# Kernel tuning notes

Hardware: AMD Instinct MI355X
Metric: run time of the kernel (lower is better)

The kernel has to match this reference:

```python
import jax, jax.numpy as jnp
import numpy as np

B, T, E = 4, 2048, 1024
H, HS = 16, 64

def setup_inputs() -> dict:
    key = jax.random.key(0)
    ks = jax.random.split(key, 6)
    return {
        "x": jax.random.normal(ks[0], (B, T, E), dtype=jnp.float32),
        "Wq": jax.random.normal(ks[1], (H, E, HS), dtype=jnp.float32) * 0.02,
        "Wk": jax.random.normal(ks[2], (H, E, HS), dtype=jnp.float32) * 0.02,
        "Wv": jax.random.normal(ks[3], (H, E, HS), dtype=jnp.float32) * 0.02,
        "proj_w": jax.random.normal(ks[4], (E, H * HS), dtype=jnp.float32) * 0.02,
        "proj_b": jax.random.normal(ks[5], (E,), dtype=jnp.float32) * 0.02,
    }

def reference(x, Wq, Wk, Wv, proj_w, proj_b):
    b, t, e = x.shape
    h, _, hs = Wq.shape
    # NOTE: original uses .view() (raw reshape, not transpose) from [b,t,h,hs]
    # to [h,b,t,hs]; we replicate that exactly for faithfulness.
    q = jnp.einsum('bxy,iyk->bxik', x, Wq).reshape(h, b, t, hs)
    k = jnp.einsum('bxy,iyk->bxik', x, Wk).reshape(h, b, t, hs)
    v = jnp.einsum('bxy,iyk->bxik', x, Wv).reshape(h, b, t, hs)
    # scores: [h, b, t, t], scaled by 1/sqrt(head_size)
    wei = jnp.einsum('hbqd,hbkd->hbqk', q, k) * (hs ** -0.5)
    causal = jnp.tril(jnp.ones((t, t), dtype=bool))  # [t, t]
    wei = jnp.where(causal, wei, -jnp.inf)
    wei = jax.nn.softmax(wei, axis=-1)  # dropout is identity in eval
    out = jnp.einsum('hbqk,hbkd->hbqd', wei, v)
    # raw reshape [h,b,t,hs] -> [b,t,h*hs], matching torch .view()
    out = out.reshape(b, t, h * hs)
    out = out @ proj_w.T + proj_b  # nn.Linear
    return out
```

## Files before the change

### kernel.cpp

```cpp
#include <hip/hip_runtime.h>

typedef unsigned short u16;
typedef __attribute__((ext_vector_type(8))) __bf16 bf16x8;
typedef __attribute__((ext_vector_type(4))) float f32x4;
typedef __attribute__((ext_vector_type(16))) float f32x16;
typedef __attribute__((ext_vector_type(4))) unsigned short ushort4v;
typedef __attribute__((ext_vector_type(2))) unsigned uint2v;

__device__ __forceinline__ u16 f2bf(float f) {
  unsigned u = __builtin_bit_cast(unsigned, f);
  u += 0x7fffu + ((u >> 16) & 1u);
  return (u16)(u >> 16);
}

__device__ __forceinline__ float exp2_hw(float x) {
  float r; asm("v_exp_f32 %0, %1" : "=v"(r) : "v"(x)); return r;
}
__device__ __forceinline__ unsigned cvt_pk_bf16(float a, float b) {
  unsigned r; asm("v_cvt_pk_bf16_f32 %0, %1, %2" : "=v"(r) : "v"(a), "v"(b)); return r;
}

__device__ __forceinline__ void gload_lds16(const void* g, void* l) {
  __builtin_amdgcn_global_load_lds(
      (__attribute__((address_space(1))) void*)g,
      (__attribute__((address_space(3))) void*)l, 16, 0, 0);
}

__device__ __forceinline__ void BAR() {
  asm volatile("" ::: "memory");
  __builtin_amdgcn_s_barrier();
  asm volatile("" ::: "memory");
}

#define MFMA16(a, b, c) __builtin_amdgcn_mfma_f32_16x16x32_bf16(a, b, c, 0, 0, 0)
#define MFMA32(a, b, c) __builtin_amdgcn_mfma_f32_32x32x16_bf16(a, b, c, 0, 0, 0)

#define QSCALE 0.1803368801111204f


__global__ __launch_bounds__(256)
void prep_kernel(const float* __restrict__ x, const float* __restrict__ Wq,
                 const float* __restrict__ Wk, const float* __restrict__ Wv,
                 const float* __restrict__ pw, u16* __restrict__ Xb,
                 u16* __restrict__ Wcat, u16* __restrict__ PWt) {
  const int b = blockIdx.x, tid = threadIdx.x;
  if (b < 8192) {
    int i = b * 256 + tid;
    float4 v = ((const float4*)x)[i];
    union { u16 u[4]; uint2 v2; } r;
    r.u[0] = f2bf(v.x); r.u[1] = f2bf(v.y); r.u[2] = f2bf(v.z); r.u[3] = f2bf(v.w);
    ((uint2*)Xb)[i] = r.v2;
  } else if (b < 8960) {
    __shared__ u16 lds[64 * 68];
    int bb = b - 8192;
    int sel = bb >> 8, rem = bb & 255;
    int h = rem >> 4, e0 = (rem & 15) * 64;
    const float* W = (sel == 0) ? Wq : (sel == 1) ? Wk : Wv;
    const float* src = W + ((size_t)h * 1024 + e0) * 64;
#pragma unroll
    for (int i = 0; i < 4; i++) {
      int idx = i * 1024 + tid * 4;
      int e = idx >> 6, hs = idx & 63;
      float4 v = *(const float4*)&src[idx];
      u16* d = &lds[e * 68 + hs];
      d[0] = f2bf(v.x); d[1] = f2bf(v.y); d[2] = f2bf(v.z); d[3] = f2bf(v.w);
    }
    __syncthreads();
#pragma unroll
    for (int i = 0; i < 2; i++) {
      int u = i * 256 + tid;
      int hs = u >> 3, ec = u & 7;
      union { u16 q[8]; uint4 v; } ou;
#pragma unroll
      for (int e = 0; e < 8; e++) ou.q[e] = lds[(ec * 8 + e) * 68 + hs];
      size_t n = (size_t)sel * 1024 + h * 64 + hs;
      *(uint4*)&Wcat[n * 1024 + e0 + ec * 8] = ou.v;
    }
  } else {
    int i = (b - 8960) * 256 + tid;
    float4 v = ((const float4*)pw)[i];
    union { u16 u[4]; uint2 v2; } r;
    r.u[0] = f2bf(v.x); r.u[1] = f2bf(v.y); r.u[2] = f2bf(v.z); r.u[3] = f2bf(v.w);
    ((uint2*)PWt)[i] = r.v2;
  }
}


template<int OUT_BF16>
__global__ __launch_bounds__(512, 2)
void gemm3b(const u16* __restrict__ A, const u16* __restrict__ BT,
            void* __restrict__ Cout, const float* __restrict__ bias,
            int M, int N, int K, int qcols) {
  __shared__ u16 a_lds[3][128 * 64];
  __shared__ u16 b_lds[3][256 * 64];
  const int xcd = blockIdx.x & 7;
  const int local = blockIdx.x >> 3;
  const int by = xcd * 8 + (local & 7);
  const int bx = local >> 3;
  const int tid = threadIdx.x;
  const int lane = tid & 63;
  const int w = tid >> 6;
  const int wr = w >> 2, wc = w & 3;
  const int mBase = by * 128, nBase = bx * 256;
  const int l15 = lane & 15, l4 = lane >> 4;
  const int nkt = K >> 6;

  f32x4 acc[4][4] = {};

  auto STAGE_A = [&](int s, int kt) {
#pragma unroll
    for (int j = 0; j < 2; j++) {
      int e = j * 4096 + tid * 8;
      int row = e >> 6;
      int c = ((e >> 3) & 7) ^ (row & 7);
      gload_lds16(A + (size_t)(mBase + row) * K + kt * 64 + c * 8, &a_lds[s][e]);
    }
  };
  auto STAGE_B = [&](int s, int kt) {
#pragma unroll
    for (int j = 0; j < 4; j++) {
      int e = j * 4096 + tid * 8;
      int row = e >> 6;
      int c = ((e >> 3) & 7) ^ (row & 7);
      gload_lds16(BT + (size_t)(nBase + row) * K + kt * 64 + c * 8, &b_lds[s][e]);
    }
  };

  STAGE_A(0, 0); STAGE_B(0, 0);
  STAGE_A(1, 1); STAGE_B(1, 1);
  asm volatile("s_waitcnt vmcnt(6)" ::: "memory");
  BAR();

  int s0 = 0, s1 = 1, s2 = 2;
  for (int t = 0; t < nkt; t++) {
    const int t2 = (t + 2 < nkt) ? t + 2 : t + 2 - nkt;
    bf16x8 AF[4][2], BF[2][2];

#pragma unroll
    for (int m = 0; m < 4; m++) {
      int row = wr * 64 + m * 16 + l15;
#pragma unroll
      for (int ks = 0; ks < 2; ks++) {
        int ch = (ks * 4 + l4) ^ (row & 7);
        AF[m][ks] = *(const bf16x8*)&a_lds[s0][row * 64 + ch * 8];
      }
    }
#pragma unroll
    for (int n = 0; n < 2; n++) {
      int row = wc * 64 + n * 16 + l15;
#pragma unroll
      for (int ks = 0; ks < 2; ks++) {
        int ch = (ks * 4 + l4) ^ (row & 7);
        BF[n][ks] = *(const bf16x8*)&b_lds[s0][row * 64 + ch * 8];
      }
    }
    STAGE_A(s2, t2);
    BAR();
    __builtin_amdgcn_s_setprio(1);
#pragma unroll
    for (int m = 0; m < 4; m++)
#pragma unroll
      for (int n = 0; n < 2; n++) {
        acc[m][n] = MFMA16(AF[m][0], BF[n][0], acc[m][n]);
        acc[m][n] = MFMA16(AF[m][1], BF[n][1], acc[m][n]);
      }
    __builtin_amdgcn_s_setprio(0);

#pragma unroll
    for (int n = 0; n < 2; n++) {
      int row = wc * 64 + 32 + n * 16 + l15;
#pragma unroll
      for (int ks = 0; ks < 2; ks++) {
        int ch = (ks * 4 + l4) ^ (row & 7);
        BF[n][ks] = *(const bf16x8*)&b_lds[s0][row * 64 + ch * 8];
      }
    }
    STAGE_B(s2, t2);
    BAR();
    __builtin_amdgcn_s_setprio(1);
#pragma unroll
    for (int m = 0; m < 4; m++)
#pragma unroll
      for (int n = 0; n < 2; n++) {
        acc[m][2 + n] = MFMA16(AF[m][0], BF[n][0], acc[m][2 + n]);
        acc[m][2 + n] = MFMA16(AF[m][1], BF[n][1], acc[m][2 + n]);
      }
    __builtin_amdgcn_s_setprio(0);

    asm volatile("s_waitcnt vmcnt(6)" ::: "memory");
    BAR();
    int tmp = s0; s0 = s1; s1 = s2; s2 = tmp;
  }

#pragma unroll
  for (int mi = 0; mi < 4; mi++) {
    int row = mBase + wr * 64 + mi * 16 + l4 * 4;
#pragma unroll
    for (int ni = 0; ni < 4; ni++) {
      int col = nBase + wc * 64 + ni * 16 + l15;
      float scl = (col < qcols) ? QSCALE : 1.f;
#pragma unroll
      for (int j = 0; j < 4; j++) {
        float v = acc[mi][ni][j];
        if (OUT_BF16) {
          ((u16*)Cout)[(size_t)(row + j) * N + col] = f2bf(v * scl);
        } else {
          ((float*)Cout)[(size_t)(row + j) * N + col] = v + bias[col];
        }
      }
    }
  }
}


__global__ __launch_bounds__(256)
void vt_build(const u16* __restrict__ qkv, u16* __restrict__ vt) {
  __shared__ u16 lds[64 * 66];
  const int hb = blockIdx.x >> 5, tc = blockIdx.x & 31;
  const int t0 = tc * 64, tid = threadIdx.x;
#pragma unroll
  for (int i = 0; i < 2; i++) {
    int idx = i * 2048 + tid * 8;
    int tl = idx >> 6, d0 = idx & 63;
    int r = hb * 2048 + t0 + tl;
    const u16* src = &qkv[(size_t)(r >> 4) * 3072 + 2048 + (r & 15) * 64 + d0];
    uint4 v = *(const uint4*)src;
    u16* dst = &lds[tl * 66 + d0];
    *(unsigned*)(dst + 0) = v.x; *(unsigned*)(dst + 2) = v.y;
    *(unsigned*)(dst + 4) = v.z; *(unsigned*)(dst + 6) = v.w;
  }
  __syncthreads();
#pragma unroll
  for (int i = 0; i < 2; i++) {
    int idx = i * 2048 + tid * 8;
    int d = idx >> 6, tl0 = idx & 63;
    union { u16 u[8]; uint4 v; } ou;
#pragma unroll
    for (int e = 0; e < 8; e++) ou.u[e] = lds[(tl0 + e) * 66 + d];
    *(uint4*)&vt[(size_t)hb * 131072 + (size_t)d * 2048 + t0 + tl0] = ou.v;
  }
}


__global__ __launch_bounds__(256)
void attn_kernel(const u16* __restrict__ qkv, const u16* __restrict__ vtg,
                 u16* __restrict__ att) {
  __shared__ u16 k_lds[2][64 * 64];
  __shared__ u16 v_lds[2][64 * 64];

  const int xcd = blockIdx.x & 7;
  const int c = blockIdx.x >> 3;
  const int hb = xcd * 8 + (c & 7);
  const int qb = 15 - (c >> 3);
  const int tid = threadIdx.x;
  const int lane = tid & 63, w = tid >> 6;
  const int l31 = lane & 31, l5 = lane >> 5;
  const int qbase = qb * 128 + w * 32;
  const int nkt = 2 * qb + 2;

  bf16x8 qf[4];
  {
    int t = qbase + l31;
    int r = hb * 2048 + t;
    size_t base = (size_t)(r >> 4) * 3072 + (r & 15) * 64;
#pragma unroll
    for (int d = 0; d < 4; d++)
      qf[d] = *(const bf16x8*)&qkv[base + d * 16 + l5 * 8];
  }

  f32x16 o0 = {}, o1 = {};
  float lp = 0.f;

  auto STAGE = [&](int buf, int kt) {
#pragma unroll
    for (int i = 0; i < 2; i++) {
      int U = i * 2048 + tid * 8;
      int row = U >> 6;
      int chunk = ((U >> 3) & 7) ^ (row & 7);
      int rK = hb * 2048 + kt * 64 + row;
      gload_lds16(&qkv[(size_t)(rK >> 4) * 3072 + 1024 + (rK & 15) * 64 + chunk * 8],
                  &k_lds[buf][U]);
    }
#pragma unroll
    for (int i = 0; i < 2; i++) {
      int U = i * 2048 + tid * 8;
      int row = U >> 6;
      int chunk = ((U >> 3) & 7) ^ (row & 7);
      gload_lds16(&vtg[(size_t)hb * 131072 + (size_t)row * 2048 + kt * 64 + chunk * 8],
                  &v_lds[buf][U]);
    }
  };

  STAGE(0, 0);
  asm volatile("s_waitcnt vmcnt(0)" ::: "memory");
  BAR();

  for (int kt = 0; kt < nkt; kt++) {
    if (kt + 1 < nkt) STAGE((kt + 1) & 1, kt + 1);
    const int cur = kt & 1;
    const bool active = (kt * 64 <= qbase + 31);
    if (active) {
      const bool full = (kt * 64 + 63 <= qbase);
      const int q = qbase + l31;
#pragma unroll
      for (int kb = 0; kb < 2; kb++) {
        int krow = kb * 32 + l31;
        int ksw = krow & 7;
        f32x16 st = {};
        __builtin_amdgcn_s_setprio(1);
#pragma unroll
        for (int t = 0; t < 4; t++) {
          bf16x8 kf = *(const bf16x8*)&k_lds[cur][krow * 64 + ((t * 2 + l5) ^ ksw) * 8];
          st = MFMA32(kf, qf[t], st);
        }
        __builtin_amdgcn_s_setprio(0);
        float p[16];
#pragma unroll
        for (int r = 0; r < 16; r++) {
          float v = st[r];
          if (!full) {
            int k = kt * 64 + kb * 32 + (r & 3) + 8 * (r >> 2) + 4 * l5;
            v = (k > q) ? -INFINITY : v;
          }
          p[r] = exp2_hw(v);
          lp += p[r];
        }
#pragma unroll
        for (int kc = 0; kc < 2; kc++) {
          unsigned w0 = cvt_pk_bf16(p[kc * 8 + 0], p[kc * 8 + 1]);
          unsigned w1 = cvt_pk_bf16(p[kc * 8 + 2], p[kc * 8 + 3]);
          unsigned w2 = cvt_pk_bf16(p[kc * 8 + 4], p[kc * 8 + 5]);
          unsigned w3 = cvt_pk_bf16(p[kc * 8 + 6], p[kc * 8 + 7]);
          uint2v sw0 = __builtin_amdgcn_permlane32_swap(w0, w2, false, false);
          uint2v sw1 = __builtin_amdgcn_permlane32_swap(w1, w3, false, false);
          union { unsigned u[4]; bf16x8 v; } pf;
          pf.u[0] = sw0.x; pf.u[1] = sw1.x; pf.u[2] = sw0.y; pf.u[3] = sw1.y;
          __builtin_amdgcn_s_setprio(1);
          {
            int row0 = l31;
            int ch0 = (kb * 4 + kc * 2 + l5) ^ (row0 & 7);
            bf16x8 vf0 = *(const bf16x8*)&v_lds[cur][row0 * 64 + ch0 * 8];
            o0 = MFMA32(vf0, pf.v, o0);
            int row1 = 32 + l31;
            int ch1 = (kb * 4 + kc * 2 + l5) ^ (row1 & 7);
            bf16x8 vf1 = *(const bf16x8*)&v_lds[cur][row1 * 64 + ch1 * 8];
            o1 = MFMA32(vf1, pf.v, o1);
          }
          __builtin_amdgcn_s_setprio(0);
        }
      }
    }
    asm volatile("s_waitcnt vmcnt(0)" ::: "memory");
    BAR();
  }

  lp += __shfl_xor(lp, 32);
  float rl = 1.f / lp;
  {
    int q = qbase + l31;
    size_t rbase = ((size_t)hb * 2048 + q) * 64;
#pragma unroll
    for (int g = 0; g < 4; g++) {
      uint2 wv;
      wv.x = cvt_pk_bf16(o0[4 * g + 0] * rl, o0[4 * g + 1] * rl);
      wv.y = cvt_pk_bf16(o0[4 * g + 2] * rl, o0[4 * g + 3] * rl);
      *(uint2*)&att[rbase + g * 8 + 4 * l5] = wv;
      uint2 wu;
      wu.x = cvt_pk_bf16(o1[4 * g + 0] * rl, o1[4 * g + 1] * rl);
      wu.y = cvt_pk_bf16(o1[4 * g + 2] * rl, o1[4 * g + 3] * rl);
      *(uint2*)&att[rbase + 32 + g * 8 + 4 * l5] = wu;
    }
  }
}


extern "C" void kernel_launch(void* const* d_in, const int* in_sizes, int n_in,
                              void* d_out, int out_size, void* d_ws, size_t ws_size,
                              hipStream_t stream) {
  const float* x  = (const float*)d_in[0];
  const float* Wq = (const float*)d_in[1];
  const float* Wk = (const float*)d_in[2];
  const float* Wv = (const float*)d_in[3];
  const float* pw = (const float*)d_in[4];
  const float* pb = (const float*)d_in[5];
  float* out = (float*)d_out;

  char* ws = (char*)d_ws;
  u16* Xb   = (u16*)(ws);
  u16* VTg  = (u16*)(ws);
  u16* Wcat = (u16*)(ws + (16u << 20));
  u16* PWt  = (u16*)(ws + (22u << 20));
  u16* QKV  = (u16*)(ws + (24u << 20));
  u16* ATT  = (u16*)(ws + (72u << 20));

  prep_kernel<<<9984, 256, 0, stream>>>(x, Wq, Wk, Wv, pw, Xb, Wcat, PWt);

  gemm3b<1><<<768, 512, 0, stream>>>(Xb, Wcat, QKV, nullptr, 8192, 3072, 1024, 1024);

  vt_build<<<2048, 256, 0, stream>>>(QKV, VTg);

  attn_kernel<<<1024, 256, 0, stream>>>(QKV, VTg, ATT);

  gemm3b<0><<<256, 512, 0, stream>>>(ATT, PWt, out, pb, 8192, 1024, 1024, 0);
}
```

Baseline: 161.5 us.

## Split attention KV range across two wave groups and merge partial outputs in LDS

The attention block grows from 256 to 512 threads. Each half of the waves processes half of the causal key tiles, with its own double-buffered K/V LDS staging, and the partial outputs and row sums are combined through LDS at the end. The goal is to halve the serial key-tile loop per block and add more waves to hide latency. In exchange it doubles LDS use, adds a reduction and an extra barrier, and may leave one half idle on diagonal tiles. The row-sum accumulation is also reordered into a tree sum.

```diff
diff --git a/kernel.cpp b/kernel.cpp
--- a/kernel.cpp
+++ b/kernel.cpp
@@ -242,11 +242,11 @@
 }
 
 
-__global__ __launch_bounds__(256)
+__global__ __launch_bounds__(512)
 void attn_kernel(const u16* __restrict__ qkv, const u16* __restrict__ vtg,
                  u16* __restrict__ att) {
-  __shared__ u16 k_lds[2][64 * 64];
-  __shared__ u16 v_lds[2][64 * 64];
+  __shared__ u16 k_lds[2][2][4096];
+  __shared__ u16 v_lds[2][2][4096];
 
   const int xcd = blockIdx.x & 7;
   const int c = blockIdx.x >> 3;
@@ -254,9 +254,10 @@
   const int qb = 15 - (c >> 3);
   const int tid = threadIdx.x;
   const int lane = tid & 63, w = tid >> 6;
+  const int qg = w & 3, kh = w >> 2;
   const int l31 = lane & 31, l5 = lane >> 5;
-  const int qbase = qb * 128 + w * 32;
-  const int nkt = 2 * qb + 2;
+  const int qbase = qb * 128 + qg * 32;
+  const int nh = qb + 1;
 
   bf16x8 qf[4];
   {
@@ -271,33 +272,38 @@
   f32x16 o0 = {}, o1 = {};
   float lp = 0.f;
 
-  auto STAGE = [&](int buf, int kt) {
+  auto STAGE = [&](int khx, int buf, int kt) {
+    int tl = tid & 255;
 #pragma unroll
     for (int i = 0; i < 2; i++) {
-      int U = i * 2048 + tid * 8;
+      int U = i * 2048 + tl * 8;
       int row = U >> 6;
       int chunk = ((U >> 3) & 7) ^ (row & 7);
       int rK = hb * 2048 + kt * 64 + row;
       gload_lds16(&qkv[(size_t)(rK >> 4) * 3072 + 1024 + (rK & 15) * 64 + chunk * 8],
-                  &k_lds[buf][U]);
+                  &k_lds[khx][buf][U]);
     }
 #pragma unroll
     for (int i = 0; i < 2; i++) {
-      int U = i * 2048 + tid * 8;
+      int U = i * 2048 + tl * 8;
       int row = U >> 6;
       int chunk = ((U >> 3) & 7) ^ (row & 7);
       gload_lds16(&vtg[(size_t)hb * 131072 + (size_t)row * 2048 + kt * 64 + chunk * 8],
-                  &v_lds[buf][U]);
+                  &v_lds[khx][buf][U]);
     }
   };
 
-  STAGE(0, 0);
+  if (tid < 256) STAGE(0, 0, 0); else STAGE(1, 0, nh);
   asm volatile("s_waitcnt vmcnt(0)" ::: "memory");
   BAR();
 
-  for (int kt = 0; kt < nkt; kt++) {
-    if (kt + 1 < nkt) STAGE((kt + 1) & 1, kt + 1);
-    const int cur = kt & 1;
+  for (int s = 0; s < nh; s++) {
+    if (s + 1 < nh) {
+      if (tid < 256) STAGE(0, (s + 1) & 1, s + 1);
+      else           STAGE(1, (s + 1) & 1, nh + s + 1);
+    }
+    const int cur = s & 1;
+    const int kt = kh ? nh + s : s;
     const bool active = (kt * 64 <= qbase + 31);
     if (active) {
       const bool full = (kt * 64 + 63 <= qbase);
@@ -310,7 +316,7 @@
         __builtin_amdgcn_s_setprio(1);
 #pragma unroll
         for (int t = 0; t < 4; t++) {
-          bf16x8 kf = *(const bf16x8*)&k_lds[cur][krow * 64 + ((t * 2 + l5) ^ ksw) * 8];
+          bf16x8 kf = *(const bf16x8*)&k_lds[kh][cur][krow * 64 + ((t * 2 + l5) ^ ksw) * 8];
           st = MFMA32(kf, qf[t], st);
         }
         __builtin_amdgcn_s_setprio(0);
@@ -323,8 +329,10 @@
             v = (k > q) ? -INFINITY : v;
           }
           p[r] = exp2_hw(v);
-          lp += p[r];
         }
+        float ps = ((p[0] + p[1]) + (p[2] + p[3])) + ((p[4] + p[5]) + (p[6] + p[7]));
+        ps += ((p[8] + p[9]) + (p[10] + p[11])) + ((p[12] + p[13]) + (p[14] + p[15]));
+        lp += ps;
 #pragma unroll
         for (int kc = 0; kc < 2; kc++) {
           unsigned w0 = cvt_pk_bf16(p[kc * 8 + 0], p[kc * 8 + 1]);
@@ -339,11 +347,11 @@
           {
             int row0 = l31;
             int ch0 = (kb * 4 + kc * 2 + l5) ^ (row0 & 7);
-            bf16x8 vf0 = *(const bf16x8*)&v_lds[cur][row0 * 64 + ch0 * 8];
+            bf16x8 vf0 = *(const bf16x8*)&v_lds[kh][cur][row0 * 64 + ch0 * 8];
             o0 = MFMA32(vf0, pf.v, o0);
             int row1 = 32 + l31;
             int ch1 = (kb * 4 + kc * 2 + l5) ^ (row1 & 7);
-            bf16x8 vf1 = *(const bf16x8*)&v_lds[cur][row1 * 64 + ch1 * 8];
+            bf16x8 vf1 = *(const bf16x8*)&v_lds[kh][cur][row1 * 64 + ch1 * 8];
             o1 = MFMA32(vf1, pf.v, o1);
           }
           __builtin_amdgcn_s_setprio(0);
@@ -354,9 +362,22 @@
     BAR();
   }
 
-  lp += __shfl_xor(lp, 32);
-  float rl = 1.f / lp;
-  {
+  float* fo = (float*)&k_lds[0][0][0];
+  float* fl = (float*)&v_lds[0][0][0];
+  if (kh == 1) {
+    float* dst = fo + ((qg * 64 + lane) << 5);
+#pragma unroll
+    for (int r = 0; r < 16; r++) { dst[r] = o0[r]; dst[16 + r] = o1[r]; }
+    fl[qg * 64 + lane] = lp;
+  }
+  __syncthreads();
+  if (kh == 0) {
+    const float* src = fo + ((qg * 64 + lane) << 5);
+#pragma unroll
+    for (int r = 0; r < 16; r++) { o0[r] += src[r]; o1[r] += src[16 + r]; }
+    lp += fl[qg * 64 + lane];
+    lp += __shfl_xor(lp, 32);
+    float rl = 1.f / lp;
     int q = qbase + l31;
     size_t rbase = ((size_t)hb * 2048 + q) * 64;
 #pragma unroll
@@ -399,7 +420,7 @@
 
   vt_build<<<2048, 256, 0, stream>>>(QKV, VTg);
 
-  attn_kernel<<<1024, 256, 0, stream>>>(QKV, VTg, ATT);
+  attn_kernel<<<1024, 512, 0, stream>>>(QKV, VTg, ATT);
 
   gemm3b<0><<<256, 512, 0, stream>>>(ATT, PWt, out, pb, 8192, 1024, 1024, 0);
 }
```

Result: slower. 175.0 us (+8.4%).
